# Kernel tuning notes

Hardware: AMD Instinct MI355X
Metric: run time of the kernel (lower is better)

Reference implementation:

```python
import jax, jax.numpy as jnp
import numpy as np

D_IN = 3
HID = 256
N_BRANCH = 8
SKIP_IN = (4,)
CSG_TREE = [0, 1, [2, 3], [4, 5, [6, 7]]]
FLAG_CONVEX = True
BETA = 100.0
N_POINTS = 100000

# layer dims: [3, 256*7, 8]; layer whose OUTPUT feeds a skip layer emits 256-3=253
_DIMS = [D_IN] + [HID] * 7 + [N_BRANCH]


def _layer_out_dim(layer):
    if (layer + 1) in SKIP_IN:
        return _DIMS[layer + 1] - D_IN
    return _DIMS[layer + 1]


def setup_inputs() -> dict:
    key = jax.random.key(0)
    keys = jax.random.split(key, 20)
    inp = {"x": jax.random.normal(keys[0], (N_POINTS, D_IN), dtype=jnp.float32)}
    n_layers = len(_DIMS) - 1  # 8 linear layers
    for layer in range(n_layers):
        in_d = _DIMS[layer]
        out_d = _layer_out_dim(layer)
        kw = jax.random.fold_in(keys[1], layer)
        if layer == n_layers - 1:  # geometric init of last layer
            W = (np.sqrt(np.pi) / np.sqrt(in_d)
                 + 1e-5 * jax.random.normal(kw, (in_d, out_d), dtype=jnp.float32))
            b = -1.0 * jnp.ones((out_d,), dtype=jnp.float32)
        else:
            W = (np.sqrt(2.0) / np.sqrt(out_d)) * jax.random.normal(
                kw, (in_d, out_d), dtype=jnp.float32)
            b = jnp.zeros((out_d,), dtype=jnp.float32)
        inp[f"W{layer}"] = W
        inp[f"b{layer}"] = b
    return inp


def _softplus_beta(x):
    return jax.nn.softplus(BETA * x) / BETA


def _csg_combine(vals, ops, cvx_flag):
    # hard CSG tree: one-hot matmul == column gather; recursion is static (trace time)
    idxs = [v for v in ops if not isinstance(v, list)]
    cols = [vals[:, jnp.array(idxs)]]
    for v in ops:
        if isinstance(v, list):
            cols.append(_csg_combine(vals, v, not cvx_flag))
    m = jnp.concatenate(cols, axis=1)
    red = jnp.max if cvx_flag else jnp.min
    return red(m, axis=1, keepdims=True)


def _forward(x, Ws, bs):
    inp = x
    h = x
    n_layers = len(Ws)
    inv_sqrt2 = np.float32(1.0 / np.sqrt(2.0))
    for layer in range(n_layers):
        if layer in SKIP_IN:
            h = jnp.concatenate([h, inp], axis=-1) * inv_sqrt2
        h = h @ Ws[layer] + bs[layer]
        if layer < n_layers - 1:
            h = _softplus_beta(h)
    branch_vals = h  # [N, n_branch]
    hcsg = _csg_combine(branch_vals, CSG_TREE, FLAG_CONVEX)  # [N, 1]
    return jnp.concatenate([hcsg, branch_vals], axis=1)  # flag_output == 0


def reference(x, W0, b0, W1, b1, W2, b2, W3, b3, W4, b4, W5, b5, W6, b6, W7, b7):
    Ws = [W0, W1, W2, W3, W4, W5, W6, W7]
    bs = [b0, b1, b2, b3, b4, b5, b6, b7]
    return _forward(x, Ws, bs)
```

## Files before the change

kernel.cpp:

```cpp
#include <hip/hip_runtime.h>
#include <hip/hip_bf16.h>


using bf16x8 = __attribute__((ext_vector_type(8))) __bf16;
using f32x4  = __attribute__((ext_vector_type(4))) float;

#define LDA 264

#define OFFW0 0
#define OFFW1 8192
#define OFFW7 401408
#define WSB_BYTE_OFF 811008
#define OFFB7 1792

#define SCALE_T2 144.26950408889634f
#define INV_SQRT2 0.70710678118654752f
#define LN2_100 0.0069314718055994531f

__device__ __forceinline__ float fast_exp2(float x) {
#if __has_builtin(__builtin_amdgcn_exp2f)
    return __builtin_amdgcn_exp2f(x);
#else
    return exp2f(x);
#endif
}

__device__ __forceinline__ float softplus_t2(float t2) {
    float e = fast_exp2(-fabsf(t2));
    float p = __builtin_fmaf(e, 0.20568f, -0.64838f);
    p = __builtin_fmaf(e, p, 1.4427f);
    return fmaxf(t2, 0.0f) + e * p;
}

__device__ __forceinline__ unsigned short bf16_rne(float f) {
    unsigned int u = __float_as_uint(f);
    unsigned int r = u + 0x7FFFu + ((u >> 16) & 1u);
    return (unsigned short)(r >> 16);
}

template <int KK, int NTG>
__device__ __forceinline__ void mfma_group(
    const unsigned short* __restrict__ wfrag,
    const float* __restrict__ bias,
    const unsigned short* act,
    f32x4 (&acc)[2][NTG], int wave, int lane)
{
    const int quad = lane >> 4;
    const int l15  = lane & 15;

#pragma unroll
    for (int i = 0; i < 2; ++i) {
        const int chb = (wave * 2 + i) * 16 + quad * 4;
        const float4 b4 = *(const float4*)(bias + chb);
#pragma unroll
        for (int nt = 0; nt < NTG; ++nt)
            acc[i][nt] = f32x4{b4.x, b4.y, b4.z, b4.w};
    }

    const unsigned short* wbase = wfrag + (wave * 2 * KK * 64 + lane) * 8;

#pragma unroll
    for (int kk = 0; kk < KK; ++kk) {
        bf16x8 bfr[NTG];
#pragma unroll
        for (int nt = 0; nt < NTG; ++nt)
            bfr[nt] = *(const bf16x8*)(act + (nt * 16 + l15) * LDA + kk * 32 + quad * 8);
#pragma unroll
        for (int i = 0; i < 2; ++i) {
            bf16x8 afr = *(const bf16x8*)(wbase + (i * KK + kk) * 512);
#pragma unroll
            for (int nt = 0; nt < NTG; ++nt)
                acc[i][nt] = __builtin_amdgcn_mfma_f32_16x16x32_bf16(afr, bfr[nt], acc[i][nt], 0, 0, 0);
        }
    }
}

template <int NTG>
__device__ __forceinline__ void epi_group_full(
    f32x4 (&acc)[2][NTG], unsigned short* act, const float* xst,
    int wave, int lane, bool splice)
{
    const int quad = lane >> 4;
    const int l15  = lane & 15;
#pragma unroll
    for (int i = 0; i < 2; ++i) {
        const int chb = (wave * 2 + i) * 16 + quad * 4;
#pragma unroll
        for (int nt = 0; nt < NTG; ++nt) {
            const int pt = nt * 16 + l15;
            float vv[4];
#pragma unroll
            for (int r = 0; r < 4; ++r)
                vv[r] = softplus_t2(acc[i][nt][r]);
            if (splice && chb == 252) {
                vv[1] = xst[pt * 4 + 0];
                vv[2] = xst[pt * 4 + 1];
                vv[3] = xst[pt * 4 + 2];
            }
            __hip_bfloat162 p01 = __float22bfloat162_rn(float2{vv[0], vv[1]});
            __hip_bfloat162 p23 = __float22bfloat162_rn(float2{vv[2], vv[3]});
            uint2 pk;
            pk.x = *(unsigned int*)&p01;
            pk.y = *(unsigned int*)&p23;
            *(uint2*)(act + pt * LDA + chb) = pk;
        }
    }
}

template <int KK, int NTG>
__device__ __forceinline__ void stag_region(
    const unsigned short* __restrict__ wfrag,
    const float* __restrict__ bias,
    const unsigned short* __restrict__ actX,
    unsigned short* actY,
    f32x4 (&accX)[2][NTG], f32x4 (&accY)[2][NTG],
    const float* xstY, bool splice, int wave, int lane)
{
    const int quad = lane >> 4;
    const int l15  = lane & 15;

#pragma unroll
    for (int i = 0; i < 2; ++i) {
        const int chb = (wave * 2 + i) * 16 + quad * 4;
        const float4 b4 = *(const float4*)(bias + chb);
#pragma unroll
        for (int nt = 0; nt < NTG; ++nt)
            accX[i][nt] = f32x4{b4.x, b4.y, b4.z, b4.w};
    }

    const unsigned short* wbase = wfrag + (wave * 2 * KK * 64 + lane) * 8;

#pragma unroll
    for (int kk = 0; kk < KK; ++kk) {
        bf16x8 bfr[NTG];
#pragma unroll
        for (int nt = 0; nt < NTG; ++nt)
            bfr[nt] = *(const bf16x8*)(actX + (nt * 16 + l15) * LDA + kk * 32 + quad * 8);

        bf16x8 a0 = *(const bf16x8*)(wbase + kk * 512);
        bf16x8 a1 = *(const bf16x8*)(wbase + (KK + kk) * 512);

        if (kk < 2 * NTG) {
            const int i  = kk & 1;
            const int nt = kk >> 1;
            const int chb = (wave * 2 + i) * 16 + quad * 4;
            const int pt  = nt * 16 + l15;
            float vv[4];
#pragma unroll
            for (int r = 0; r < 4; ++r)
                vv[r] = softplus_t2(accY[i][nt][r]);
            if (splice && chb == 252) {
                vv[1] = xstY[pt * 4 + 0];
                vv[2] = xstY[pt * 4 + 1];
                vv[3] = xstY[pt * 4 + 2];
            }
            __hip_bfloat162 p01 = __float22bfloat162_rn(float2{vv[0], vv[1]});
            __hip_bfloat162 p23 = __float22bfloat162_rn(float2{vv[2], vv[3]});
            uint2 pk;
            pk.x = *(unsigned int*)&p01;
            pk.y = *(unsigned int*)&p23;
            *(uint2*)(actY + pt * LDA + chb) = pk;
        }

#pragma unroll
        for (int nt = 0; nt < NTG; ++nt)
            accX[0][nt] = __builtin_amdgcn_mfma_f32_16x16x32_bf16(a0, bfr[nt], accX[0][nt], 0, 0, 0);
#pragma unroll
        for (int nt = 0; nt < NTG; ++nt)
            accX[1][nt] = __builtin_amdgcn_mfma_f32_16x16x32_bf16(a1, bfr[nt], accX[1][nt], 0, 0, 0);
    }
}

__device__ __forceinline__ void l7_part(
    const unsigned short* act, const unsigned short* __restrict__ w7,
    const float* __restrict__ wsB, float* __restrict__ out,
    int row0, int ptg0, int npts, int lane)
{
    const int quad = lane >> 4, l15 = lane & 15;
    const float4 b4 = *(const float4*)(wsB + OFFB7 + quad * 4);
    f32x4 acc = f32x4{b4.x, b4.y, b4.z, b4.w};
#pragma unroll
    for (int kk = 0; kk < 8; ++kk) {
        bf16x8 bfr = *(const bf16x8*)(act + (row0 + l15) * LDA + kk * 32 + quad * 8);
        bf16x8 afr = *(const bf16x8*)(w7 + (kk * 64 + lane) * 8);
        acc = __builtin_amdgcn_mfma_f32_16x16x32_bf16(afr, bfr, acc, 0, 0, 0);
    }
    float u0 = __shfl(acc[0], l15 + 16);
    float u1 = __shfl(acc[1], l15 + 16);
    float u2 = __shfl(acc[2], l15 + 16);
    float u3 = __shfl(acc[3], l15 + 16);
    if (quad == 0) {
        const int ptg = ptg0 + l15;
        if (ptg < npts) {
            const float v0 = acc[0], v1 = acc[1], v2 = acc[2], v3 = acc[3];
            const float v4 = u0, v5 = u1, v6 = u2, v7 = u3;
            const float m23   = fminf(v2, v3);
            const float m67   = fmaxf(v6, v7);
            const float m4567 = fminf(fminf(v4, v5), m67);
            const float h     = fmaxf(fmaxf(v0, v1), fmaxf(m23, m4567));
            float* o = out + (long)ptg * 9;
            o[0] = h;
            o[1] = v0; o[2] = v1; o[3] = v2; o[4] = v3;
            o[5] = v4; o[6] = v5; o[7] = v6; o[8] = v7;
        }
    }
}

template <int NTG>
__device__ __forceinline__ void run_net(
    const float* __restrict__ x, float* __restrict__ out,
    const unsigned short* __restrict__ wsW, const float* __restrict__ wsB,
    unsigned short* act, float* xst,
    int base_pt, int npts, int tid)
{
    const int wave = tid >> 6, lane = tid & 63;

    for (int i = tid; i < 2 * NTG * 16 * 32; i += 512) {
        const int pt = i >> 5, ch = i & 31;
        const int ptg = base_pt + pt;
        float v = 0.0f;
        if (ch < 3 && ptg < npts) v = x[ptg * 3 + ch];
        act[pt * LDA + ch] = bf16_rne(v);
        if (ch < 4) xst[pt * 4 + ch] = (ch < 3) ? v : 0.0f;
    }
    __syncthreads();

    unsigned short* actA = act;
    unsigned short* actB = act + NTG * 16 * LDA;
    const float* xstA = xst;
    const float* xstB = xst + NTG * 16 * 4;

    f32x4 accA[2][NTG], accB[2][NTG];

    mfma_group<1, NTG>(wsW + OFFW0, wsB, actA, accA, wave, lane);
    __syncthreads();
    mfma_group<1, NTG>(wsW + OFFW0, wsB, actB, accB, wave, lane);
    epi_group_full<NTG>(accA, actA, xstA, wave, lane, false);
    __syncthreads();

#pragma unroll 1
    for (int l = 1; l <= 6; ++l) {
        const unsigned short* Wl = wsW + OFFW1 + (l - 1) * 65536;
        const float* bl = wsB + l * 256;

        stag_region<8, NTG>(Wl, bl, actA, actB, accA, accB, xstB, l == 4, wave, lane);
        __syncthreads();

        stag_region<8, NTG>(Wl, bl, actB, actA, accB, accA, xstA, l == 3, wave, lane);
        __syncthreads();
    }

    if (wave < NTG)
        l7_part(act, wsW + OFFW7, wsB, out, wave * 16, base_pt + wave * 16, npts, lane);
    epi_group_full<NTG>(accB, actB, xstB, wave, lane, false);
    __syncthreads();

    if (wave < NTG)
        l7_part(act, wsW + OFFW7, wsB, out,
                NTG * 16 + wave * 16, base_pt + NTG * 16 + wave * 16, npts, lane);
}

__global__ __launch_bounds__(512, 4)
void nhrep_main(const float* __restrict__ x, float* __restrict__ out,
                const unsigned short* __restrict__ wsW,
                const float* __restrict__ wsB, int npts, int nbig)
{
    __shared__ unsigned short act[96 * LDA];
    __shared__ float xst[96 * 4];
    const int b = blockIdx.x;
    if (b < nbig) {
        run_net<3>(x, out, wsW, wsB, act, xst, b * 96, npts, threadIdx.x);
    } else {
        run_net<1>(x, out, wsW, wsB, act, xst,
                   nbig * 96 + (b - nbig) * 32, npts, threadIdx.x);
    }
}

struct PackArgs {
    const float* W[8];
    const float* b[8];
};

#define TOTAL_FRAGS 50688
#define TOTAL_BIAS  1808

__global__ void prepack_all(PackArgs args, unsigned short* __restrict__ dstW,
                            float* __restrict__ dstB)
{
    const int t = blockIdx.x * blockDim.x + threadIdx.x;
    const int FB[9]  = {0, 1024, 9216, 17408, 25600, 33792, 41984, 50176, 50688};
    const int KKs[8] = {1, 8, 8, 8, 8, 8, 8, 8};
    const int ind[8] = {3, 256, 256, 256, 256, 256, 256, 256};
    const int outd[8]= {256, 256, 256, 253, 256, 256, 256, 8};

    if (t < TOTAL_FRAGS) {
        int l = 0;
        while (t >= FB[l + 1]) ++l;
        const int f    = t - FB[l];
        const int lane = f & 63;
        const int kk   = (f >> 6) % KKs[l];
        const int mt   = f / (64 * KKs[l]);
        const int o    = mt * 16 + (lane & 15);
        const int kb   = kk * 32 + (lane >> 4) * 8;
        const float* W = args.W[l];
        const int in_d = ind[l], out_d = outd[l];

        unsigned short v[8];
#pragma unroll
        for (int j = 0; j < 8; ++j) {
            const int k = kb + j;
            float w = 0.0f;
            if (k < in_d && o < out_d) {
                float sc = 1.0f;
                if (l == 0) sc = SCALE_T2;
                else if (l == 4) sc = (k < 253) ? INV_SQRT2 : (SCALE_T2 * INV_SQRT2);
                else if (l == 7) sc = LN2_100;
                w = W[k * out_d + o] * sc;
            }
            unsigned int u = __float_as_uint(w);
            v[j] = (unsigned short)((u + 0x7FFFu + ((u >> 16) & 1u)) >> 16);
        }
        uint4 p;
        p.x = (unsigned int)v[0] | ((unsigned int)v[1] << 16);
        p.y = (unsigned int)v[2] | ((unsigned int)v[3] << 16);
        p.z = (unsigned int)v[4] | ((unsigned int)v[5] << 16);
        p.w = (unsigned int)v[6] | ((unsigned int)v[7] << 16);
        *(uint4*)(dstW + (long)t * 8) = p;
    } else if (t < TOTAL_FRAGS + TOTAL_BIAS) {
        const int u = t - TOTAL_FRAGS;
        const int l = (u < 1792) ? (u >> 8) : 7;
        const int idx = (l < 7) ? (u & 255) : (u - 1792);
        const float sc = (l < 7) ? SCALE_T2 : 1.0f;
        dstB[u] = (idx < outd[l]) ? args.b[l][idx] * sc : 0.0f;
    }
}

extern "C" void kernel_launch(void* const* d_in, const int* in_sizes, int n_in,
                              void* d_out, int out_size, void* d_ws, size_t ws_size,
                              hipStream_t stream)
{
    const float* x = (const float*)d_in[0];
    unsigned short* wsW = (unsigned short*)d_ws;
    float* wsB = (float*)((char*)d_ws + WSB_BYTE_OFF);

    PackArgs pa;
    for (int l = 0; l < 8; ++l) {
        pa.W[l] = (const float*)d_in[1 + 2 * l];
        pa.b[l] = (const float*)d_in[2 + 2 * l];
    }
    const int ptot = TOTAL_FRAGS + TOTAL_BIAS;
    prepack_all<<<(ptot + 255) / 256, 256, 0, stream>>>(pa, wsW, wsB);

    const int npts = in_sizes[0] / 3;
    int nbig, nsmall;
    const int tail_pts = 16384;
    if (npts > tail_pts) {
        nbig = (npts - tail_pts + 95) / 96;
        const int base_small = nbig * 96;
        nsmall = (npts - base_small + 31) / 32;
    } else {
        nbig = 0;
        nsmall = (npts + 31) / 32;
    }
    nhrep_main<<<nbig + nsmall, 512, 0, stream>>>(x, (float*)d_out, wsW, wsB,
                                                  npts, nbig);
}
```

Measured before the change: 184.9 us.

## Retile waves as 4 channel groups by 2 point halves with asymmetric A/B halves

Waves now split work 4 channel-groups by 2 point-halves, each wave computing 4 output tiles of 16 channels over NT point tiles, instead of every wave covering all points for 2 channel tiles. The two ping-pong halves can hold different sizes (2 and 1 tiles per wave for the 96-point blocks), and tail blocks now process 64 points instead of 32. The aim is to cut redundant LDS activation reads per wave and let each weight fragment feed more MFMAs. The cost is more weight-fragment loads per activation reuse and uneven stagger work between the two halves. The l7 gating also changes, so up to 4 waves handle the output layer.

```diff
diff --git a/kernel.cpp b/kernel.cpp
--- a/kernel.cpp
+++ b/kernel.cpp
@@ -38,56 +38,59 @@
     return (unsigned short)(r >> 16);
 }
 
-template <int KK, int NTG>
+
+template <int KK, int NT>
 __device__ __forceinline__ void mfma_group(
     const unsigned short* __restrict__ wfrag,
     const float* __restrict__ bias,
     const unsigned short* act,
-    f32x4 (&acc)[2][NTG], int wave, int lane)
+    f32x4 (&acc)[4][NT], int c, int p, int lane)
 {
     const int quad = lane >> 4;
     const int l15  = lane & 15;
-
-#pragma unroll
-    for (int i = 0; i < 2; ++i) {
-        const int chb = (wave * 2 + i) * 16 + quad * 4;
+    const int row0 = p * NT * 16 + l15;
+
+#pragma unroll
+    for (int i = 0; i < 4; ++i) {
+        const int chb = (c * 4 + i) * 16 + quad * 4;
         const float4 b4 = *(const float4*)(bias + chb);
 #pragma unroll
-        for (int nt = 0; nt < NTG; ++nt)
+        for (int nt = 0; nt < NT; ++nt)
             acc[i][nt] = f32x4{b4.x, b4.y, b4.z, b4.w};
     }
 
-    const unsigned short* wbase = wfrag + (wave * 2 * KK * 64 + lane) * 8;
+    const unsigned short* wbase = wfrag + (c * 4 * KK * 64 + lane) * 8;
 
 #pragma unroll
     for (int kk = 0; kk < KK; ++kk) {
-        bf16x8 bfr[NTG];
-#pragma unroll
-        for (int nt = 0; nt < NTG; ++nt)
-            bfr[nt] = *(const bf16x8*)(act + (nt * 16 + l15) * LDA + kk * 32 + quad * 8);
-#pragma unroll
-        for (int i = 0; i < 2; ++i) {
-            bf16x8 afr = *(const bf16x8*)(wbase + (i * KK + kk) * 512);
-#pragma unroll
-            for (int nt = 0; nt < NTG; ++nt)
-                acc[i][nt] = __builtin_amdgcn_mfma_f32_16x16x32_bf16(afr, bfr[nt], acc[i][nt], 0, 0, 0);
-        }
-    }
-}
-
-template <int NTG>
+        bf16x8 bfr[NT];
+#pragma unroll
+        for (int nt = 0; nt < NT; ++nt)
+            bfr[nt] = *(const bf16x8*)(act + (row0 + nt * 16) * LDA + kk * 32 + quad * 8);
+#pragma unroll
+        for (int i = 0; i < 4; ++i) {
+            bf16x8 a = *(const bf16x8*)(wbase + (i * KK + kk) * 512);
+#pragma unroll
+            for (int nt = 0; nt < NT; ++nt)
+                acc[i][nt] = __builtin_amdgcn_mfma_f32_16x16x32_bf16(a, bfr[nt], acc[i][nt], 0, 0, 0);
+        }
+    }
+}
+
+template <int NT>
 __device__ __forceinline__ void epi_group_full(
-    f32x4 (&acc)[2][NTG], unsigned short* act, const float* xst,
-    int wave, int lane, bool splice)
+    f32x4 (&acc)[4][NT], unsigned short* act, const float* xst,
+    int c, int p, int lane, bool splice)
 {
     const int quad = lane >> 4;
     const int l15  = lane & 15;
-#pragma unroll
-    for (int i = 0; i < 2; ++i) {
-        const int chb = (wave * 2 + i) * 16 + quad * 4;
-#pragma unroll
-        for (int nt = 0; nt < NTG; ++nt) {
-            const int pt = nt * 16 + l15;
+    const int row0 = p * NT * 16 + l15;
+#pragma unroll
+    for (int i = 0; i < 4; ++i) {
+        const int chb = (c * 4 + i) * 16 + quad * 4;
+#pragma unroll
+        for (int nt = 0; nt < NT; ++nt) {
+            const int pt = row0 + nt * 16;
             float vv[4];
 #pragma unroll
             for (int r = 0; r < 4; ++r)
@@ -107,44 +110,43 @@
     }
 }
 
-template <int KK, int NTG>
+template <int KK, int NTX, int NTY>
 __device__ __forceinline__ void stag_region(
     const unsigned short* __restrict__ wfrag,
     const float* __restrict__ bias,
     const unsigned short* __restrict__ actX,
     unsigned short* actY,
-    f32x4 (&accX)[2][NTG], f32x4 (&accY)[2][NTG],
-    const float* xstY, bool splice, int wave, int lane)
+    f32x4 (&accX)[4][NTX], f32x4 (&accY)[4][NTY],
+    const float* xstY, bool splice, int c, int p, int lane)
 {
     const int quad = lane >> 4;
     const int l15  = lane & 15;
-
-#pragma unroll
-    for (int i = 0; i < 2; ++i) {
-        const int chb = (wave * 2 + i) * 16 + quad * 4;
+    const int rowX0 = p * NTX * 16 + l15;
+    const int rowY0 = p * NTY * 16 + l15;
+
+#pragma unroll
+    for (int i = 0; i < 4; ++i) {
+        const int chb = (c * 4 + i) * 16 + quad * 4;
         const float4 b4 = *(const float4*)(bias + chb);
 #pragma unroll
-        for (int nt = 0; nt < NTG; ++nt)
+        for (int nt = 0; nt < NTX; ++nt)
             accX[i][nt] = f32x4{b4.x, b4.y, b4.z, b4.w};
     }
 
-    const unsigned short* wbase = wfrag + (wave * 2 * KK * 64 + lane) * 8;
+    const unsigned short* wbase = wfrag + (c * 4 * KK * 64 + lane) * 8;
 
 #pragma unroll
     for (int kk = 0; kk < KK; ++kk) {
-        bf16x8 bfr[NTG];
-#pragma unroll
-        for (int nt = 0; nt < NTG; ++nt)
-            bfr[nt] = *(const bf16x8*)(actX + (nt * 16 + l15) * LDA + kk * 32 + quad * 8);
-
-        bf16x8 a0 = *(const bf16x8*)(wbase + kk * 512);
-        bf16x8 a1 = *(const bf16x8*)(wbase + (KK + kk) * 512);
-
-        if (kk < 2 * NTG) {
-            const int i  = kk & 1;
-            const int nt = kk >> 1;
-            const int chb = (wave * 2 + i) * 16 + quad * 4;
-            const int pt  = nt * 16 + l15;
+        bf16x8 bfr[NTX];
+#pragma unroll
+        for (int nt = 0; nt < NTX; ++nt)
+            bfr[nt] = *(const bf16x8*)(actX + (rowX0 + nt * 16) * LDA + kk * 32 + quad * 8);
+
+        if (kk < 4 * NTY) {
+            const int i  = kk & 3;
+            const int nt = kk >> 2;
+            const int chb = (c * 4 + i) * 16 + quad * 4;
+            const int pt  = rowY0 + nt * 16;
             float vv[4];
 #pragma unroll
             for (int r = 0; r < 4; ++r)
@@ -163,11 +165,12 @@
         }
 
 #pragma unroll
-        for (int nt = 0; nt < NTG; ++nt)
-            accX[0][nt] = __builtin_amdgcn_mfma_f32_16x16x32_bf16(a0, bfr[nt], accX[0][nt], 0, 0, 0);
-#pragma unroll
-        for (int nt = 0; nt < NTG; ++nt)
-            accX[1][nt] = __builtin_amdgcn_mfma_f32_16x16x32_bf16(a1, bfr[nt], accX[1][nt], 0, 0, 0);
+        for (int i = 0; i < 4; ++i) {
+            bf16x8 a = *(const bf16x8*)(wbase + (i * KK + kk) * 512);
+#pragma unroll
+            for (int nt = 0; nt < NTX; ++nt)
+                accX[i][nt] = __builtin_amdgcn_mfma_f32_16x16x32_bf16(a, bfr[nt], accX[i][nt], 0, 0, 0);
+        }
     }
 }
 
@@ -206,7 +209,7 @@
     }
 }
 
-template <int NTG>
+template <int NTA, int NTB>
 __device__ __forceinline__ void run_net(
     const float* __restrict__ x, float* __restrict__ out,
     const unsigned short* __restrict__ wsW, const float* __restrict__ wsB,
@@ -214,8 +217,12 @@
     int base_pt, int npts, int tid)
 {
     const int wave = tid >> 6, lane = tid & 63;
-
-    for (int i = tid; i < 2 * NTG * 16 * 32; i += 512) {
+    const int c = wave >> 1, p = wave & 1;
+    constexpr int HA = 2 * NTA * 16;
+    constexpr int HB = 2 * NTB * 16;
+    constexpr int TP = HA + HB;
+
+    for (int i = tid; i < TP * 32; i += 512) {
         const int pt = i >> 5, ch = i & 31;
         const int ptg = base_pt + pt;
         float v = 0.0f;
@@ -226,16 +233,16 @@
     __syncthreads();
 
     unsigned short* actA = act;
-    unsigned short* actB = act + NTG * 16 * LDA;
+    unsigned short* actB = act + HA * LDA;
     const float* xstA = xst;
-    const float* xstB = xst + NTG * 16 * 4;
-
-    f32x4 accA[2][NTG], accB[2][NTG];
-
-    mfma_group<1, NTG>(wsW + OFFW0, wsB, actA, accA, wave, lane);
+    const float* xstB = xst + HA * 4;
+
+    f32x4 accA[4][NTA], accB[4][NTB];
+
+    mfma_group<1, NTA>(wsW + OFFW0, wsB, actA, accA, c, p, lane);
     __syncthreads();
-    mfma_group<1, NTG>(wsW + OFFW0, wsB, actB, accB, wave, lane);
-    epi_group_full<NTG>(accA, actA, xstA, wave, lane, false);
+    mfma_group<1, NTB>(wsW + OFFW0, wsB, actB, accB, c, p, lane);
+    epi_group_full<NTA>(accA, actA, xstA, c, p, lane, false);
     __syncthreads();
 
 #pragma unroll 1
@@ -243,21 +250,24 @@
         const unsigned short* Wl = wsW + OFFW1 + (l - 1) * 65536;
         const float* bl = wsB + l * 256;
 
-        stag_region<8, NTG>(Wl, bl, actA, actB, accA, accB, xstB, l == 4, wave, lane);
+        stag_region<8, NTA, NTB>(Wl, bl, actA, actB, accA, accB, xstB,
+                                 l == 4, c, p, lane);
         __syncthreads();
 
-        stag_region<8, NTG>(Wl, bl, actB, actA, accB, accA, xstA, l == 3, wave, lane);
+        stag_region<8, NTB, NTA>(Wl, bl, actB, actA, accB, accA, xstA,
+                                 l == 3, c, p, lane);
         __syncthreads();
     }
 
-    if (wave < NTG)
-        l7_part(act, wsW + OFFW7, wsB, out, wave * 16, base_pt + wave * 16, npts, lane);
-    epi_group_full<NTG>(accB, actB, xstB, wave, lane, false);
+    if (wave < 2 * NTA)
+        l7_part(act, wsW + OFFW7, wsB, out, wave * 16, base_pt + wave * 16,
+                npts, lane);
+    epi_group_full<NTB>(accB, actB, xstB, c, p, lane, false);
     __syncthreads();
 
-    if (wave < NTG)
+    if (wave < 2 * NTB)
         l7_part(act, wsW + OFFW7, wsB, out,
-                NTG * 16 + wave * 16, base_pt + NTG * 16 + wave * 16, npts, lane);
+                HA + wave * 16, base_pt + HA + wave * 16, npts, lane);
 }
 
 __global__ __launch_bounds__(512, 4)
@@ -269,10 +279,10 @@
     __shared__ float xst[96 * 4];
     const int b = blockIdx.x;
     if (b < nbig) {
-        run_net<3>(x, out, wsW, wsB, act, xst, b * 96, npts, threadIdx.x);
+        run_net<2, 1>(x, out, wsW, wsB, act, xst, b * 96, npts, threadIdx.x);
     } else {
-        run_net<1>(x, out, wsW, wsB, act, xst,
-                   nbig * 96 + (b - nbig) * 32, npts, threadIdx.x);
+        run_net<1, 1>(x, out, wsW, wsB, act, xst,
+                      nbig * 96 + (b - nbig) * 64, npts, threadIdx.x);
     }
 }
 
@@ -357,10 +367,10 @@
     if (npts > tail_pts) {
         nbig = (npts - tail_pts + 95) / 96;
         const int base_small = nbig * 96;
-        nsmall = (npts - base_small + 31) / 32;
+        nsmall = (npts - base_small + 63) / 64;
     } else {
         nbig = 0;
-        nsmall = (npts + 31) / 32;
+        nsmall = (npts + 63) / 64;
     }
     nhrep_main<<<nbig + nsmall, 512, 0, stream>>>(x, (float*)d_out, wsW, wsB,
                                                   npts, nbig);
```

Result: slower. 492.8 us (+166.5%).
